# Kernel tuning notes

Hardware: AMD Instinct MI355X
Metric: run time of the kernel (lower is better)

The kernel has to match this reference:

```python
import jax, jax.numpy as jnp
import numpy as np

N = 100000
E = 600000
G = 8
HID = 128
HEADS = 4
C = HID // HEADS  # 32


def setup_inputs() -> dict:
    key = jax.random.key(0)
    ks = jax.random.split(key, 32)
    s = 0.05
    node_numeric = jax.random.normal(ks[0], (N, 8), jnp.float32)
    node_cat0 = jax.random.randint(ks[1], (N,), 0, 32)
    node_cat1 = jax.random.randint(ks[2], (N,), 0, 64)
    edge_numeric = jax.random.normal(ks[3], (E, 4), jnp.float32)
    edge_cat0 = jax.random.randint(ks[4], (E,), 0, 16)
    edge_cat1 = jax.random.randint(ks[5], (E,), 0, 100)
    src = jax.random.randint(ks[6], (E,), 0, N)
    dst = jax.random.randint(ks[7], (E,), 0, N)
    dst = jnp.where(dst == src, (dst + 1) % N, dst)  # GATConv removes self-loops before adding its own
    edge_index = jnp.stack([src, dst])
    batch = jnp.sort(jax.random.randint(ks[8], (N,), 0, G))
    recipe = jax.random.normal(ks[9], (G, 16), jnp.float32)
    return dict(
        node_numeric=node_numeric, node_cat0=node_cat0, node_cat1=node_cat1,
        edge_numeric=edge_numeric, edge_cat0=edge_cat0, edge_cat1=edge_cat1,
        edge_index=edge_index, batch=batch, recipe=recipe,
        emb_node0=jax.random.normal(ks[10], (32, 6), jnp.float32) * s,
        emb_node1=jax.random.normal(ks[11], (64, 8), jnp.float32) * s,
        emb_edge0=jax.random.normal(ks[12], (16, 4), jnp.float32) * s,
        emb_edge1=jax.random.normal(ks[13], (100, 10), jnp.float32) * s,
        W_in=jax.random.normal(ks[14], (38, HID), jnp.float32) * s,
        b_in=jnp.zeros((HID,), jnp.float32),
        W_edge=jax.random.normal(ks[15], (18, HID), jnp.float32) * s,
        b_edge=jnp.zeros((HID,), jnp.float32),
        gat_lin=jax.random.normal(ks[16], (3, HID, HID), jnp.float32) * s,
        gat_lin_edge=jax.random.normal(ks[17], (3, HID, HID), jnp.float32) * s,
        att_src=jax.random.normal(ks[18], (3, HEADS, C), jnp.float32) * s,
        att_dst=jax.random.normal(ks[19], (3, HEADS, C), jnp.float32) * s,
        att_edge=jax.random.normal(ks[20], (3, HEADS, C), jnp.float32) * s,
        gat_bias=jnp.zeros((3, HID), jnp.float32),
        W_r1=jax.random.normal(ks[21], (HID, HID), jnp.float32) * s,
        b_r1=jnp.zeros((HID,), jnp.float32),
        W_r2=jax.random.normal(ks[22], (HID, 1), jnp.float32) * s,
        b_r2=jnp.zeros((1,), jnp.float32),
    )


def _segment_softmax(logits, seg, num):
    m = jax.ops.segment_max(logits, seg, num_segments=num)
    ex = jnp.exp(logits - m[seg])
    s = jax.ops.segment_sum(ex, seg, num_segments=num)
    return ex / s[seg]


def _forward(node_numeric, edge_numeric, recipe,
             emb_node0, emb_node1, emb_edge0, emb_edge1,
             W_in, b_in, W_edge, b_edge,
             gat_lin, gat_lin_edge, att_src, att_dst, att_edge, gat_bias,
             W_r1, b_r1, W_r2, b_r2,
             node_cat0, node_cat1, edge_cat0, edge_cat1, edge_index, batch):
    n = node_numeric.shape[0]
    src, dst = edge_index[0], edge_index[1]
    # node encoding: numeric + categorical embeddings + broadcast recipe
    h = jnp.concatenate([node_numeric, emb_node0[node_cat0], emb_node1[node_cat1], recipe[batch]], axis=1)
    h = jax.nn.relu(h @ W_in + b_in)
    # edge encoding (shared across GAT layers)
    e = jnp.concatenate([edge_numeric, emb_edge0[edge_cat0], emb_edge1[edge_cat1]], axis=1)
    e = e @ W_edge + b_edge
    # self-loops with fill_value='mean': per-dst mean of incoming edge_attr
    cnt = jax.ops.segment_sum(jnp.ones((e.shape[0],), e.dtype), dst, num_segments=n)
    loop = jax.ops.segment_sum(e, dst, num_segments=n) / jnp.maximum(cnt, 1.0)[:, None]
    ar = jnp.arange(n)
    src_a = jnp.concatenate([src, ar])
    dst_a = jnp.concatenate([dst, ar])
    e_a = jnp.concatenate([e, loop], axis=0)  # [E+N, HID]
    for l in range(gat_lin.shape[0]):
        x = (h @ gat_lin[l]).reshape(n, HEADS, C)          # shared lin_src/lin_dst
        ee = (e_a @ gat_lin_edge[l]).reshape(-1, HEADS, C)
        a_s = jnp.sum(x * att_src[l], axis=-1)   # [N, HEADS]
        a_d = jnp.sum(x * att_dst[l], axis=-1)
        a_e = jnp.sum(ee * att_edge[l], axis=-1)  # [E+N, HEADS]
        logits = jax.nn.leaky_relu(a_s[src_a] + a_d[dst_a] + a_e, negative_slope=0.2)
        alpha = _segment_softmax(logits, dst_a, n)  # segment softmax over dst
        out = jax.ops.segment_sum(x[src_a] * alpha[:, :, None], dst_a, num_segments=n)
        h = jax.nn.relu(out.reshape(n, HID) + gat_bias[l])  # dropout off (eval)
    g = jax.ops.segment_sum(h, batch, num_segments=G)  # global_add_pool
    g = jax.nn.relu(g @ W_r1 + b_r1)
    return g @ W_r2 + b_r2  # [G, 1]


def reference(node_numeric, node_cat0, node_cat1, edge_numeric, edge_cat0, edge_cat1,
              edge_index, batch, recipe,
              emb_node0, emb_node1, emb_edge0, emb_edge1,
              W_in, b_in, W_edge, b_edge,
              gat_lin, gat_lin_edge, att_src, att_dst, att_edge, gat_bias,
              W_r1, b_r1, W_r2, b_r2):
    return _forward(node_numeric, edge_numeric, recipe,
                    emb_node0, emb_node1, emb_edge0, emb_edge1,
                    W_in, b_in, W_edge, b_edge,
                    gat_lin, gat_lin_edge, att_src, att_dst, att_edge, gat_bias,
                    W_r1, b_r1, W_r2, b_r2,
                    node_cat0, node_cat1, edge_cat0, edge_cat1, edge_index, batch)
```

## Files before the change

### kernel.cpp

```cpp
#include <hip/hip_runtime.h>
#include <math.h>

#define HID 128

typedef float f32x4 __attribute__((ext_vector_type(4)));
typedef short bf16x8 __attribute__((ext_vector_type(8)));
typedef unsigned int uint32;

__device__ __forceinline__ float leaky02(float z) { return z >= 0.f ? z : 0.2f * z; }
__device__ __forceinline__ unsigned short f2bf(float f) {
  uint32 u = __float_as_uint(f);
  u = (u + 0x7fff + ((u >> 16) & 1)) >> 16;
  return (unsigned short)u;
}
__device__ __forceinline__ float bf2f(uint32 us) { return __uint_as_float(us << 16); }
__device__ __forceinline__ float bflo(uint32 w) { return __uint_as_float(w << 16); }
__device__ __forceinline__ float bfhi(uint32 w) { return __uint_as_float(w & 0xffff0000u); }

__global__ void k_enc(const float* __restrict__ nodenum, const int* __restrict__ c0,
                      const int* __restrict__ c1, const int* __restrict__ batch,
                      const float* __restrict__ recipe,
                      const float* __restrict__ e0, const float* __restrict__ e1,
                      const float* __restrict__ Win, const float* __restrict__ bin,
                      unsigned short* __restrict__ hb, int n) {
  __shared__ float f[8][40];
  __shared__ int idx[8][3];
  int t = threadIdx.x;
  int col = t & 127;
  int half = t >> 7;
  float w[40];
#pragma unroll
  for (int k = 0; k < 38; k++) w[k] = Win[k * 128 + col];
  w[38] = 0.f;
  w[39] = 0.f;
  float bias = bin[col];
  int ntiles = (n + 7) / 8;
  for (int tile = blockIdx.x; tile < ntiles; tile += gridDim.x) {
    int base = tile * 8;
    if (t < 64) {
      int r = t >> 3, k = t & 7;
      int v = base + r;
      f[r][k] = (v < n) ? nodenum[(size_t)v * 8 + k] : 0.f;
    } else if (t < 88) {
      int j = t - 64;
      int r = j / 3, which = j - r * 3;
      int v = base + r;
      int val = 0;
      if (v < n) val = (which == 0) ? c0[v] : ((which == 1) ? c1[v] : batch[v]);
      idx[r][which] = val;
    } else if (t >= 240) {
      int r = t - 240;
      if (r < 8) { f[r][38] = 0.f; f[r][39] = 0.f; }
    }
    __syncthreads();
    if (t < 240) {
      int r = t / 30, k = t - r * 30;
      float val;
      if (k < 6) val = e0[idx[r][0] * 6 + k];
      else if (k < 14) val = e1[idx[r][1] * 8 + (k - 6)];
      else val = recipe[idx[r][2] * 16 + (k - 14)];
      f[r][8 + k] = val;
    }
    __syncthreads();
#pragma unroll
    for (int rr = 0; rr < 4; rr++) {
      int r = half * 4 + rr;
      int v = base + r;
      float acc = bias;
#pragma unroll
      for (int k4 = 0; k4 < 10; k4++) {
        float4 fv = *(const float4*)(&f[r][k4 * 4]);
        acc += fv.x * w[k4 * 4] + fv.y * w[k4 * 4 + 1] + fv.z * w[k4 * 4 + 2] +
               fv.w * w[k4 * 4 + 3];
      }
      if (v < n) hb[(size_t)v * 128 + col] = f2bf(fmaxf(acc, 0.f));
    }
    __syncthreads();
  }
}

__global__ void k_prep(const float* __restrict__ gle, const float* __restrict__ atte,
                       const float* __restrict__ We, const float* __restrict__ be,
                       float* __restrict__ P, float* __restrict__ q) {
  __shared__ float M[512];
  int l = blockIdx.x;
  int t = threadIdx.x;
#pragma unroll
  for (int i = 0; i < 2; i++) {
    int idx = t + i * 256;
    int k = idx >> 2, hh = idx & 3;
    float acc = 0.f;
    for (int c = 0; c < 32; c++)
      acc += gle[l * 16384 + k * 128 + hh * 32 + c] * atte[l * 128 + hh * 32 + c];
    M[k * 4 + hh] = acc;
  }
  __syncthreads();
  if (t < 72) {
    int j = t >> 2, hh = t & 3;
    float acc = 0.f;
    for (int k = 0; k < 128; k++) acc += We[j * 128 + k] * M[k * 4 + hh];
    P[(l * 18 + j) * 4 + hh] = acc;
  } else if (t < 76) {
    int hh = t - 72;
    float acc = 0.f;
    for (int k = 0; k < 128; k++) acc += be[k] * M[k * 4 + hh];
    q[l * 4 + hh] = acc;
  }
}

__global__ void k_wprep(const float* __restrict__ glin, unsigned short* __restrict__ WbfT) {
  int idx = blockIdx.x * 256 + threadIdx.x;
  if (idx >= 3 * 128 * 128) return;
  int l = idx >> 14;
  int rem = idx & 16383;
  int col = rem >> 7;
  int k = rem & 127;
  WbfT[idx] = f2bf(glin[(l << 14) + k * 128 + col]);
}

__global__ void k_deg(const int* __restrict__ dst, int* __restrict__ cnt, int E) {
  int i = blockIdx.x * 256 + threadIdx.x;
  if (i < E) atomicAdd(&cnt[dst[i]], 1);
}

__global__ void k_ae(const float* __restrict__ enum_, const int* __restrict__ ec0,
                     const int* __restrict__ ec1, const int* __restrict__ dst,
                     const int* __restrict__ srcarr,
                     const float* __restrict__ ee0, const float* __restrict__ ee1,
                     const float* __restrict__ P, const float* __restrict__ q,
                     int* __restrict__ cursor, unsigned short* __restrict__ rec,
                     int E) {
  __shared__ float Ps[216];
  __shared__ float qs[12];
  int t = threadIdx.x;
  for (int i = t; i < 216; i += 256) Ps[i] = P[i];
  if (t < 12) qs[t] = q[t];
  __syncthreads();
  int i = blockIdx.x * 256 + t;
  if (i >= E) return;
  float raw[18];
  float4 nm = *(const float4*)(enum_ + (size_t)i * 4);
  raw[0] = nm.x; raw[1] = nm.y; raw[2] = nm.z; raw[3] = nm.w;
  int a0 = ec0[i], a1 = ec1[i];
  float4 eb0 = *(const float4*)(ee0 + a0 * 4);
  raw[4] = eb0.x; raw[5] = eb0.y; raw[6] = eb0.z; raw[7] = eb0.w;
#pragma unroll
  for (int j = 0; j < 10; j++) raw[8 + j] = ee1[a1 * 10 + j];
  int d = dst[i];
  int pos = atomicAdd(&cursor[d], 1);
  uint32 wbuf[8];
#pragma unroll
  for (int l = 0; l < 3; l++) {
    float o[4];
#pragma unroll
    for (int hh = 0; hh < 4; hh++) {
      float acc = qs[l * 4 + hh];
#pragma unroll
      for (int j = 0; j < 18; j++) acc += raw[j] * Ps[(l * 18 + j) * 4 + hh];
      o[hh] = acc;
    }
    wbuf[l * 2] = (uint32)f2bf(o[0]) | ((uint32)f2bf(o[1]) << 16);
    wbuf[l * 2 + 1] = (uint32)f2bf(o[2]) | ((uint32)f2bf(o[3]) << 16);
  }
  wbuf[6] = (uint32)srcarr[i];
  wbuf[7] = 0;
  uint4* dp = (uint4*)(rec + (size_t)pos * 16);
  dp[0] = make_uint4(wbuf[0], wbuf[1], wbuf[2], wbuf[3]);
  dp[1] = make_uint4(wbuf[4], wbuf[5], wbuf[6], wbuf[7]);
}

__global__ void k_loopmean(const unsigned short* __restrict__ rec,
                           const int* __restrict__ rowptr,
                           float* __restrict__ aeL, int n, int E) {
  int v = blockIdx.x * 256 + threadIdx.x;
  if (v >= n) return;
  int beg = rowptr[v], end = rowptr[v + 1];
  float s[12];
#pragma unroll
  for (int m = 0; m < 12; m++) s[m] = 0.f;
  for (int j = beg; j < end; j++) {
    const uint4* rp = (const uint4*)(rec + (size_t)j * 16);
    uint4 r0 = rp[0];
    uint32 w4 = ((const uint32*)&rp[1])[0];
    uint32 w5 = ((const uint32*)&rp[1])[1];
    s[0] += bflo(r0.x); s[1] += bfhi(r0.x);
    s[2] += bflo(r0.y); s[3] += bfhi(r0.y);
    s[4] += bflo(r0.z); s[5] += bfhi(r0.z);
    s[6] += bflo(r0.w); s[7] += bfhi(r0.w);
    s[8] += bflo(w4);   s[9] += bfhi(w4);
    s[10] += bflo(w5);  s[11] += bfhi(w5);
  }
  float inv = (end > beg) ? 1.f / (float)(end - beg) : 0.f;
#pragma unroll
  for (int l = 0; l < 3; l++)
    *(float4*)(aeL + ((size_t)l * n + v) * 4) =
        make_float4(s[l * 4] * inv, s[l * 4 + 1] * inv, s[l * 4 + 2] * inv,
                    s[l * 4 + 3] * inv);
}

__global__ void k_scan1(const int* __restrict__ cnt, int* __restrict__ excl,
                        int* __restrict__ bsum, int n) {
  __shared__ int sh[256];
  int t = threadIdx.x;
  int i = blockIdx.x * 256 + t;
  int v = (i < n) ? cnt[i] : 0;
  sh[t] = v;
  __syncthreads();
  for (int off = 1; off < 256; off <<= 1) {
    int add = (t >= off) ? sh[t - off] : 0;
    __syncthreads();
    sh[t] += add;
    __syncthreads();
  }
  if (i < n) excl[i] = sh[t] - v;
  if (t == 255) bsum[blockIdx.x] = sh[255];
}

__global__ void k_scan2(int* __restrict__ bsum, int nb) {
  __shared__ int sh[512];
  int t = threadIdx.x;
  int v = (t < nb) ? bsum[t] : 0;
  sh[t] = v;
  __syncthreads();
  for (int off = 1; off < 512; off <<= 1) {
    int add = (t >= off) ? sh[t - off] : 0;
    __syncthreads();
    sh[t] += add;
    __syncthreads();
  }
  if (t < nb) bsum[t] = sh[t] - v;
}

__global__ void k_scan3(int* __restrict__ rowptr, const int* __restrict__ boff,
                        int* __restrict__ cursor, int n, int E) {
  int i = blockIdx.x * 256 + threadIdx.x;
  if (i < n) {
    int val = rowptr[i] + boff[i >> 8];
    rowptr[i] = val;
    cursor[i] = val;
  }
  if (i == 0) rowptr[n] = E;
}

__global__ void __launch_bounds__(512, 4)
k_x(const unsigned short* __restrict__ hb, const unsigned short* __restrict__ WbfT,
    const float* __restrict__ att_s, const float* __restrict__ att_d,
    unsigned short* __restrict__ xb, float* __restrict__ a_s,
    float* __restrict__ a_d, int n) {
  __shared__ unsigned short hs[64 * 128];
  int t = threadIdx.x;
  int w = t >> 6, l = t & 63;
  int ch = w >> 2, wr = w & 3;
  int lr = l & 15, lg = l >> 4;
  bf16x8 bfrag[4][4];
#pragma unroll
  for (int ct = 0; ct < 4; ct++) {
#pragma unroll
    for (int ks = 0; ks < 4; ks++) {
      int col = ch * 64 + ct * 16 + lr;
      int k0 = ks * 32 + lg * 8;
      bfrag[ct][ks] = *(const bf16x8*)(WbfT + col * 128 + k0);
    }
  }
  float avs[4], avd[4];
#pragma unroll
  for (int ct = 0; ct < 4; ct++) {
    avs[ct] = att_s[ch * 64 + ct * 16 + lr];
    avd[ct] = att_d[ch * 64 + ct * 16 + lr];
  }
  for (int tb = blockIdx.x * 64; tb < n; tb += gridDim.x * 64) {
    __syncthreads();
#pragma unroll
    for (int i = 0; i < 2; i++) {
      int idx = t + i * 512;
      int r = idx >> 4, c = idx & 15;
      uint4 vv = make_uint4(0, 0, 0, 0);
      if (tb + r < n) vv = *(const uint4*)(hb + (size_t)(tb + r) * 128 + c * 8);
      *(uint4*)(&hs[r * 128 + ((c ^ (r & 7)) * 8)]) = vv;
    }
    __syncthreads();
    f32x4 acc[4];
#pragma unroll
    for (int ct = 0; ct < 4; ct++) acc[ct] = (f32x4){0.f, 0.f, 0.f, 0.f};
#pragma unroll
    for (int ks = 0; ks < 4; ks++) {
      int r = wr * 16 + lr;
      int c = ks * 4 + lg;
      bf16x8 a = *(const bf16x8*)(&hs[r * 128 + ((c ^ (r & 7)) * 8)]);
#pragma unroll
      for (int ct = 0; ct < 4; ct++)
        acc[ct] = __builtin_amdgcn_mfma_f32_16x16x32_bf16(a, bfrag[ct][ks], acc[ct], 0, 0, 0);
    }
#pragma unroll
    for (int j = 0; j < 4; j++) {
      int row = tb + wr * 16 + lg * 4 + j;
      bool ok = row < n;
      if (ok) {
#pragma unroll
        for (int ct = 0; ct < 4; ct++)
          xb[(size_t)row * 128 + ch * 64 + ct * 16 + lr] = f2bf(acc[ct][j]);
      }
      float psA = acc[0][j] * avs[0] + acc[1][j] * avs[1];
      float pdA = acc[0][j] * avd[0] + acc[1][j] * avd[1];
      float psB = acc[2][j] * avs[2] + acc[3][j] * avs[3];
      float pdB = acc[2][j] * avd[2] + acc[3][j] * avd[3];
#pragma unroll
      for (int m = 1; m <= 8; m <<= 1) {
        psA += __shfl_xor(psA, m); pdA += __shfl_xor(pdA, m);
        psB += __shfl_xor(psB, m); pdB += __shfl_xor(pdB, m);
      }
      if (lr == 0 && ok) {
        a_s[(size_t)row * 4 + ch * 2] = psA;
        a_s[(size_t)row * 4 + ch * 2 + 1] = psB;
        a_d[(size_t)row * 4 + ch * 2] = pdA;
        a_d[(size_t)row * 4 + ch * 2 + 1] = pdB;
      }
    }
  }
}

__global__ void k_agg(const unsigned short* __restrict__ xb, const float* __restrict__ a_s,
                      const float* __restrict__ a_d, const unsigned short* __restrict__ rec,
                      const float* __restrict__ aeL,
                      const int* __restrict__ rowptr, const float* __restrict__ bias,
                      unsigned short* __restrict__ hbout, int n, int E, int l) {
  int wid = threadIdx.x >> 6;
  int v = blockIdx.x * 4 + wid;
  if (v >= n) return;
  int lane = threadIdx.x & 63;
  int el = lane >> 2;
  int hh = lane & 3;
  float ad_own = a_d[(size_t)v * 4 + hh];
  float as_own = a_s[(size_t)v * 4 + hh];
  float aeL_own = aeL[((size_t)l * n + v) * 4 + hh];
  float m_own = leaky02(as_own + ad_own + aeL_own);
  float s_own = 1.f;
  int c2 = lane * 2;
  int headO = lane >> 4;
  const char* xB = (const char*)xb;
  uint32 coff = (uint32)c2 * 2u;
  uint32 wv = *(const uint32*)(xB + ((uint32)v << 8) + coff);
  float a0 = bflo(wv);
  float a1 = bfhi(wv);
  int beg = rowptr[v], end = rowptr[v + 1];
  for (int cb = beg; cb < end; cb += 16) {
    int ne = end - cb;
    if (ne > 16) ne = 16;
    float logit = -1e30f;
    int srcE = 0;
    if (el < ne) {
      int j = cb + el;
      const unsigned short* rp = rec + (size_t)j * 16;
      srcE = *(const int*)(rp + 12);
      float aev = bf2f((uint32)rp[l * 4 + hh]);
      float asrc = a_s[(size_t)srcE * 4 + hh];
      logit = leaky02(asrc + ad_own + aev);
    }
    float cm = logit;
    cm = fmaxf(cm, __shfl_xor(cm, 4));
    cm = fmaxf(cm, __shfl_xor(cm, 8));
    cm = fmaxf(cm, __shfl_xor(cm, 16));
    cm = fmaxf(cm, __shfl_xor(cm, 32));
    float mn_own = fmaxf(m_own, cm);
    float p = (el < ne) ? __expf(logit - mn_own) : 0.f;
    float ps = p;
    ps += __shfl_xor(ps, 4);
    ps += __shfl_xor(ps, 8);
    ps += __shfl_xor(ps, 16);
    ps += __shfl_xor(ps, 32);
    float c_own = __expf(m_own - mn_own);
    m_own = mn_own;
    s_own = s_own * c_own + ps;
    float cO = __shfl(c_own, headO);
    a0 *= cO;
    a1 *= cO;
    int e = 0;
    for (; e + 2 <= ne; e += 2) {
      int se0 = __builtin_amdgcn_readlane(srcE, e * 4);
      int se1 = __builtin_amdgcn_readlane(srcE, e * 4 + 4);
      float p0 = __shfl(p, e * 4 + headO);
      float p1 = __shfl(p, e * 4 + 4 + headO);
      uint32 x0 = *(const uint32*)(xB + ((uint32)se0 << 8) + coff);
      uint32 x1 = *(const uint32*)(xB + ((uint32)se1 << 8) + coff);
      a0 += p0 * bflo(x0) + p1 * bflo(x1);
      a1 += p0 * bfhi(x0) + p1 * bfhi(x1);
    }
    if (e < ne) {
      int se = __builtin_amdgcn_readlane(srcE, e * 4);
      float pC = __shfl(p, e * 4 + headO);
      uint32 xw = *(const uint32*)(xB + ((uint32)se << 8) + coff);
      a0 += pC * bflo(xw);
      a1 += pC * bfhi(xw);
    }
  }
  float sO = __shfl(s_own, headO);
  float r0 = fmaxf(a0 / sO + bias[l * HID + c2], 0.f);
  float r1 = fmaxf(a1 / sO + bias[l * HID + c2 + 1], 0.f);
  uint32 pk = (uint32)f2bf(r0) | ((uint32)f2bf(r1) << 16);
  *(uint32*)(hbout + (size_t)v * HID + c2) = pk;
}

__global__ void k_pool(const unsigned short* __restrict__ hb, const int* __restrict__ batch,
                       float* __restrict__ g, int n) {
  int t = threadIdx.x;
  int per = (n + gridDim.x - 1) / gridDim.x;
  int start = blockIdx.x * per;
  int end = min(n, start + per);
  float acc = 0.f;
  int cur = -1;
  for (int v = start; v < end; v++) {
    int b = batch[v];
    if (b != cur) {
      if (cur >= 0) atomicAdd(&g[cur * 128 + t], acc);
      acc = 0.f;
      cur = b;
    }
    acc += bf2f((uint32)hb[(size_t)v * 128 + t]);
  }
  if (cur >= 0) atomicAdd(&g[cur * 128 + t], acc);
}

__global__ void k_head(const float* __restrict__ g, const float* __restrict__ Wr1,
                       const float* __restrict__ br1, const float* __restrict__ Wr2,
                       const float* __restrict__ br2, float* __restrict__ out, int G_) {
  __shared__ float gl[128];
  __shared__ float red[128];
  int i = blockIdx.x;
  int t = threadIdx.x;
  gl[t] = g[i * 128 + t];
  __syncthreads();
  float acc = br1[t];
  for (int k = 0; k < 128; k++) acc += gl[k] * Wr1[k * 128 + t];
  float hv = fmaxf(acc, 0.f);
  red[t] = hv * Wr2[t];
  __syncthreads();
  for (int off = 64; off >= 1; off >>= 1) {
    if (t < off) red[t] += red[t + off];
    __syncthreads();
  }
  if (t == 0) out[i] = red[0] + br2[0];
}

extern "C" void kernel_launch(void* const* d_in, const int* in_sizes, int n_in,
                              void* d_out, int out_size, void* d_ws, size_t ws_size,
                              hipStream_t stream) {
  const float* node_numeric = (const float*)d_in[0];
  const int* node_cat0 = (const int*)d_in[1];
  const int* node_cat1 = (const int*)d_in[2];
  const float* edge_numeric = (const float*)d_in[3];
  const int* edge_cat0 = (const int*)d_in[4];
  const int* edge_cat1 = (const int*)d_in[5];
  const int* edge_index = (const int*)d_in[6];
  const int* batch = (const int*)d_in[7];
  const float* recipe = (const float*)d_in[8];
  const float* emb_node0 = (const float*)d_in[9];
  const float* emb_node1 = (const float*)d_in[10];
  const float* emb_edge0 = (const float*)d_in[11];
  const float* emb_edge1 = (const float*)d_in[12];
  const float* W_in = (const float*)d_in[13];
  const float* b_in = (const float*)d_in[14];
  const float* W_edge = (const float*)d_in[15];
  const float* b_edge = (const float*)d_in[16];
  const float* gat_lin = (const float*)d_in[17];
  const float* gat_lin_edge = (const float*)d_in[18];
  const float* att_src = (const float*)d_in[19];
  const float* att_dst = (const float*)d_in[20];
  const float* att_edge = (const float*)d_in[21];
  const float* gat_bias = (const float*)d_in[22];
  const float* W_r1 = (const float*)d_in[23];
  const float* b_r1 = (const float*)d_in[24];
  const float* W_r2 = (const float*)d_in[25];
  const float* b_r2 = (const float*)d_in[26];

  int N = in_sizes[0] / 8;
  int E = in_sizes[3] / 4;
  int Gn = in_sizes[8] / 16;
  const int* srcArr = edge_index;
  const int* dstArr = edge_index + E;

  char* ws = (char*)d_ws;
  size_t o = 0;
  auto alloc = [&](size_t b) {
    char* p = ws + o;
    o = (o + b + 255) & ~(size_t)255;
    return p;
  };
  unsigned short* hbf = (unsigned short*)alloc((size_t)N * 128 * 2);
  unsigned short* xbf = (unsigned short*)alloc((size_t)N * 128 * 2);
  unsigned short* rec = (unsigned short*)alloc((size_t)E * 16 * 2);
  float* aeL = (float*)alloc((size_t)N * 12 * 4);
  float* a_s = (float*)alloc((size_t)N * 4 * 4);
  float* a_d = (float*)alloc((size_t)N * 4 * 4);
  float* P = (float*)alloc(216 * 4);
  float* q = (float*)alloc(12 * 4);
  unsigned short* WbfT = (unsigned short*)alloc(3 * 128 * 128 * 2);
  int* cnt = (int*)alloc((size_t)N * 4);
  int* rowptr = (int*)alloc((size_t)(N + 1) * 4);
  int* cursor = (int*)alloc((size_t)N * 4);
  int* bsum = (int*)alloc(512 * 4);
  float* g = (float*)alloc((size_t)Gn * 128 * 4);
  (void)ws_size;

  (void)hipMemsetAsync(cnt, 0, (size_t)N * 4, stream);
  (void)hipMemsetAsync(g, 0, (size_t)Gn * 128 * 4, stream);

  int nbl = (N + 255) / 256;
  int ebl = (E + 255) / 256;

  k_enc<<<2048, 256, 0, stream>>>(node_numeric, node_cat0, node_cat1, batch, recipe,
                                  emb_node0, emb_node1, W_in, b_in, hbf, N);
  k_prep<<<3, 256, 0, stream>>>(gat_lin_edge, att_edge, W_edge, b_edge, P, q);
  k_wprep<<<192, 256, 0, stream>>>(gat_lin, WbfT);
  k_deg<<<ebl, 256, 0, stream>>>(dstArr, cnt, E);
  k_scan1<<<nbl, 256, 0, stream>>>(cnt, rowptr, bsum, N);
  k_scan2<<<1, 512, 0, stream>>>(bsum, nbl);
  k_scan3<<<nbl, 256, 0, stream>>>(rowptr, bsum, cursor, N, E);
  k_ae<<<ebl, 256, 0, stream>>>(edge_numeric, edge_cat0, edge_cat1, dstArr, srcArr,
                                emb_edge0, emb_edge1, P, q, cursor, rec, E);
  k_loopmean<<<nbl, 256, 0, stream>>>(rec, rowptr, aeL, N, E);

  for (int l = 0; l < 3; l++) {
    k_x<<<1024, 512, 0, stream>>>(hbf, WbfT + l * 16384, att_src + l * 128,
                                  att_dst + l * 128, xbf, a_s, a_d, N);
    k_agg<<<(N + 3) / 4, 256, 0, stream>>>(xbf, a_s, a_d, rec, aeL, rowptr,
                                           gat_bias, hbf, N, E, l);
  }
  k_pool<<<1024, 128, 0, stream>>>(hbf, batch, g, N);
  k_head<<<Gn, 128, 0, stream>>>(g, W_r1, b_r1, W_r2, b_r2, (float*)d_out, Gn);
}
```

Measured before the change: 419.1 us.

## Process two destination nodes per wavefront in GAT aggregation with wider loads

```diff
diff --git a/kernel.cpp b/kernel.cpp
--- a/kernel.cpp
+++ b/kernel.cpp
@@ -325,27 +325,30 @@
                       const int* __restrict__ rowptr, const float* __restrict__ bias,
                       unsigned short* __restrict__ hbout, int n, int E, int l) {
   int wid = threadIdx.x >> 6;
-  int v = blockIdx.x * 4 + wid;
-  if (v >= n) return;
   int lane = threadIdx.x & 63;
-  int el = lane >> 2;
+  int half = lane >> 5;
+  int hl = lane & 31;
+  int v = blockIdx.x * 8 + wid * 2 + half;
+  bool act = v < n;
+  int vL = act ? v : 0;
+  int el = hl >> 2;
   int hh = lane & 3;
-  float ad_own = a_d[(size_t)v * 4 + hh];
-  float as_own = a_s[(size_t)v * 4 + hh];
-  float aeL_own = aeL[((size_t)l * n + v) * 4 + hh];
+  int hd = hl >> 3;
+  float ad_own = act ? a_d[(size_t)vL * 4 + hh] : 0.f;
+  float as_own = act ? a_s[(size_t)vL * 4 + hh] : 0.f;
+  float aeL_own = act ? aeL[((size_t)l * n + vL) * 4 + hh] : 0.f;
   float m_own = leaky02(as_own + ad_own + aeL_own);
   float s_own = 1.f;
-  int c2 = lane * 2;
-  int headO = lane >> 4;
   const char* xB = (const char*)xb;
-  uint32 coff = (uint32)c2 * 2u;
-  uint32 wv = *(const uint32*)(xB + ((uint32)v << 8) + coff);
-  float a0 = bflo(wv);
-  float a1 = bfhi(wv);
-  int beg = rowptr[v], end = rowptr[v + 1];
-  for (int cb = beg; cb < end; cb += 16) {
+  uint32 coff = (uint32)hl * 8u;
+  uint2 xw0 = *(const uint2*)(xB + ((uint32)vL << 8) + coff);
+  float a0 = bflo(xw0.x), a1 = bfhi(xw0.x), a2 = bflo(xw0.y), a3 = bfhi(xw0.y);
+  int beg = act ? rowptr[vL] : 0;
+  int end = act ? rowptr[vL + 1] : 0;
+  int hbase = lane & 32;
+  for (int cb = beg; cb < end; cb += 8) {
     int ne = end - cb;
-    if (ne > 16) ne = 16;
+    if (ne > 8) ne = 8;
     float logit = -1e30f;
     int srcE = 0;
     if (el < ne) {
@@ -360,44 +363,52 @@
     cm = fmaxf(cm, __shfl_xor(cm, 4));
     cm = fmaxf(cm, __shfl_xor(cm, 8));
     cm = fmaxf(cm, __shfl_xor(cm, 16));
-    cm = fmaxf(cm, __shfl_xor(cm, 32));
     float mn_own = fmaxf(m_own, cm);
     float p = (el < ne) ? __expf(logit - mn_own) : 0.f;
     float ps = p;
     ps += __shfl_xor(ps, 4);
     ps += __shfl_xor(ps, 8);
     ps += __shfl_xor(ps, 16);
-    ps += __shfl_xor(ps, 32);
     float c_own = __expf(m_own - mn_own);
     m_own = mn_own;
     s_own = s_own * c_own + ps;
-    float cO = __shfl(c_own, headO);
-    a0 *= cO;
-    a1 *= cO;
+    float cO = __shfl(c_own, hbase | hd);
+    a0 *= cO; a1 *= cO; a2 *= cO; a3 *= cO;
     int e = 0;
     for (; e + 2 <= ne; e += 2) {
-      int se0 = __builtin_amdgcn_readlane(srcE, e * 4);
-      int se1 = __builtin_amdgcn_readlane(srcE, e * 4 + 4);
-      float p0 = __shfl(p, e * 4 + headO);
-      float p1 = __shfl(p, e * 4 + 4 + headO);
-      uint32 x0 = *(const uint32*)(xB + ((uint32)se0 << 8) + coff);
-      uint32 x1 = *(const uint32*)(xB + ((uint32)se1 << 8) + coff);
-      a0 += p0 * bflo(x0) + p1 * bflo(x1);
-      a1 += p0 * bfhi(x0) + p1 * bfhi(x1);
+      int se0 = __shfl(srcE, hbase | (e * 4));
+      int se1 = __shfl(srcE, hbase | (e * 4 + 4));
+      float p0 = __shfl(p, hbase | (e * 4) | hd);
+      float p1 = __shfl(p, hbase | (e * 4 + 4) | hd);
+      uint2 x0 = *(const uint2*)(xB + ((uint32)se0 << 8) + coff);
+      uint2 x1 = *(const uint2*)(xB + ((uint32)se1 << 8) + coff);
+      a0 += p0 * bflo(x0.x) + p1 * bflo(x1.x);
+      a1 += p0 * bfhi(x0.x) + p1 * bfhi(x1.x);
+      a2 += p0 * bflo(x0.y) + p1 * bflo(x1.y);
+      a3 += p0 * bfhi(x0.y) + p1 * bfhi(x1.y);
     }
     if (e < ne) {
-      int se = __builtin_amdgcn_readlane(srcE, e * 4);
-      float pC = __shfl(p, e * 4 + headO);
-      uint32 xw = *(const uint32*)(xB + ((uint32)se << 8) + coff);
-      a0 += pC * bflo(xw);
-      a1 += pC * bfhi(xw);
-    }
-  }
-  float sO = __shfl(s_own, headO);
-  float r0 = fmaxf(a0 / sO + bias[l * HID + c2], 0.f);
-  float r1 = fmaxf(a1 / sO + bias[l * HID + c2 + 1], 0.f);
-  uint32 pk = (uint32)f2bf(r0) | ((uint32)f2bf(r1) << 16);
-  *(uint32*)(hbout + (size_t)v * HID + c2) = pk;
+      int se = __shfl(srcE, hbase | (e * 4));
+      float pC = __shfl(p, hbase | (e * 4) | hd);
+      uint2 xw = *(const uint2*)(xB + ((uint32)se << 8) + coff);
+      a0 += pC * bflo(xw.x);
+      a1 += pC * bfhi(xw.x);
+      a2 += pC * bflo(xw.y);
+      a3 += pC * bfhi(xw.y);
+    }
+  }
+  float sO = __shfl(s_own, hbase | hd);
+  float4 bv = *(const float4*)(bias + l * HID + hl * 4);
+  float r0 = fmaxf(a0 / sO + bv.x, 0.f);
+  float r1 = fmaxf(a1 / sO + bv.y, 0.f);
+  float r2 = fmaxf(a2 / sO + bv.z, 0.f);
+  float r3 = fmaxf(a3 / sO + bv.w, 0.f);
+  if (act) {
+    uint2 pk;
+    pk.x = (uint32)f2bf(r0) | ((uint32)f2bf(r1) << 16);
+    pk.y = (uint32)f2bf(r2) | ((uint32)f2bf(r3) << 16);
+    *(uint2*)(hbout + (size_t)vL * HID + hl * 4) = pk;
+  }
 }
 
 __global__ void k_pool(const unsigned short* __restrict__ hb, const int* __restrict__ batch,
@@ -522,7 +533,7 @@
   for (int l = 0; l < 3; l++) {
     k_x<<<1024, 512, 0, stream>>>(hbf, WbfT + l * 16384, att_src + l * 128,
                                   att_dst + l * 128, xbf, a_s, a_d, N);
-    k_agg<<<(N + 3) / 4, 256, 0, stream>>>(xbf, a_s, a_d, rec, aeL, rowptr,
+    k_agg<<<(N + 7) / 8, 256, 0, stream>>>(xbf, a_s, a_d, rec, aeL, rowptr,
                                            gat_bias, hbf, N, E, l);
   }
   k_pool<<<1024, 128, 0, stream>>>(hbf, batch, g, N);
```

New measurement: 384.0 us. 1.09x faster.
